# Kernel tuning notes

Measured on AMD Instinct MI355X. Metric: run time of the kernel, lower is better.

## Reference

```python
import jax, jax.numpy as jnp
import numpy as np

LN_EPS = 1e-5


def setup_inputs() -> dict:
    key = jax.random.key(0)
    ks = jax.random.split(key, 6)
    N, E, D = 100000, 600000, 128
    x = jax.random.normal(ks[0], (N, D), dtype=jnp.float32)
    edge_index = jax.random.randint(ks[1], (2, E), 0, N, dtype=jnp.int64)
    dropout_mask = jax.random.uniform(ks[2], (N, D), dtype=jnp.float32)
    ln_gamma = jnp.ones((D,), dtype=jnp.float32)
    ln_beta = jnp.zeros((D,), dtype=jnp.float32)
    W_l = jax.random.normal(ks[3], (D, D), dtype=jnp.float32) / np.sqrt(D)
    b_l = jnp.zeros((D,), dtype=jnp.float32)
    W_r = jax.random.normal(ks[4], (D, D), dtype=jnp.float32) / np.sqrt(D)
    return {"x": x, "edge_index": edge_index, "dropout_mask": dropout_mask,
            "ln_gamma": ln_gamma, "ln_beta": ln_beta,
            "W_l": W_l, "b_l": b_l, "W_r": W_r}


def reference(x, edge_index, dropout_mask, ln_gamma, ln_beta, W_l, b_l, W_r):
    N = x.shape[0]
    # LayerNorm (elementwise affine) -> ReLU -> dropout mask
    mu = jnp.mean(x, axis=-1, keepdims=True)
    var = jnp.mean(jnp.square(x - mu), axis=-1, keepdims=True)
    h = (x - mu) * jax.lax.rsqrt(var + LN_EPS) * ln_gamma + ln_beta
    h = jax.nn.relu(h) * dropout_mask  # [N, D]
    # SAGEConv with mean aggregation: messages flow src -> dst
    src, dst = edge_index[0], edge_index[1]
    agg = jax.ops.segment_sum(h[src], dst, num_segments=N)  # [N, D]
    cnt = jax.ops.segment_sum(jnp.ones_like(dst, dtype=h.dtype), dst,
                              num_segments=N)
    mean_agg = agg / jnp.maximum(cnt, 1.0)[:, None]
    # out = lin_l(mean_agg) + lin_r(h); PyG stores weights as [out, in]
    return mean_agg @ W_l.T + b_l + h @ W_r.T
```

## Files before the change

### kernel.cpp

```cpp
#include <hip/hip_runtime.h>

#define LN_EPS 1e-5f
#define D 128
#define SCAN_CHUNK 1024
#define LDSA_STRIDE 264

typedef __attribute__((ext_vector_type(4))) float f32x4;
typedef __attribute__((ext_vector_type(8))) short bf16x8;

static __device__ __forceinline__ ushort f2bf(float f) {
    union { float f; unsigned u; } a; a.f = f;
    unsigned r = a.u + 0x7FFF + ((a.u >> 16) & 1);
    return (ushort)(r >> 16);
}
static __device__ __forceinline__ float bf2f(ushort u) {
    union { unsigned u; float f; } a; a.u = ((unsigned)u) << 16;
    return a.f;
}

__global__ void prep_w(const float* __restrict__ Wl,
                       const float* __restrict__ Wr,
                       ushort* __restrict__ Bfrag,
                       int* __restrict__ hist, int N) {
    int t = blockIdx.x * blockDim.x + threadIdx.x;
    if (t < 8 * 8 * 64 * 8) {
        int i    = t & 7;
        int lane = (t >> 3) & 63;
        int jb   = (t >> 9) & 7;
        int ks   = t >> 12;
        int k = ks * 32 + (lane >> 4) * 8 + i;
        int j = jb * 16 + (lane & 15);
        float v = (k < D) ? Wl[j * D + k] : Wr[j * D + (k - D)];
        Bfrag[t] = f2bf(v);
    }
    for (int i = t; i < N; i += gridDim.x * blockDim.x) hist[i] = 0;
}

__global__ void ln_hist(const float* __restrict__ x,
                        const float* __restrict__ mask,
                        const float* __restrict__ gamma,
                        const float* __restrict__ beta,
                        ushort* __restrict__ hbf,
                        const int* __restrict__ ei,
                        int* __restrict__ hist,
                        int N, int E, int histBlocks) {
    if ((int)blockIdx.x < histBlocks) {
        int e = blockIdx.x * blockDim.x + threadIdx.x;
        if (e < E) atomicAdd(&hist[ei[E + e]], 1);
        return;
    }
    int lane = threadIdx.x & 63;
    int wid  = (((int)blockIdx.x - histBlocks) * (int)blockDim.x + (int)threadIdx.x) >> 6;
    int node = wid * 2 + (lane >> 5);
    if (node >= N) return;
    int sl = lane & 31;
    f32x4 v = ((const f32x4*)(x + (size_t)node * D))[sl];
    float s  = v.x + v.y + v.z + v.w;
    float ss = v.x * v.x + v.y * v.y + v.z * v.z + v.w * v.w;
#pragma unroll
    for (int off = 16; off > 0; off >>= 1) {
        s  += __shfl_xor(s, off);
        ss += __shfl_xor(ss, off);
    }
    float mu  = s * (1.0f / D);
    float var = ss * (1.0f / D) - mu * mu;
    float rs  = rsqrtf(var + LN_EPS);
    f32x4 g = ((const f32x4*)gamma)[sl];
    f32x4 b = ((const f32x4*)beta)[sl];
    f32x4 m = ((const f32x4*)(mask + (size_t)node * D))[sl];
    ushort4 o;
    o.x = f2bf(fmaxf((v.x - mu) * rs * g.x + b.x, 0.0f) * m.x);
    o.y = f2bf(fmaxf((v.y - mu) * rs * g.y + b.y, 0.0f) * m.y);
    o.z = f2bf(fmaxf((v.z - mu) * rs * g.z + b.z, 0.0f) * m.z);
    o.w = f2bf(fmaxf((v.w - mu) * rs * g.w + b.w, 0.0f) * m.w);
    ((ushort4*)(hbf + (size_t)node * D))[sl] = o;
}

__global__ void scan1(const int* __restrict__ hist, int* __restrict__ offs,
                      int* __restrict__ chunk_sums, int N) {
    __shared__ int lds[256];
    int base = blockIdx.x * SCAN_CHUNK;
    int t = threadIdx.x;
    int idx0 = base + t * 4;
    int v[4];
#pragma unroll
    for (int i = 0; i < 4; i++) {
        int idx = idx0 + i;
        v[i] = (idx < N) ? hist[idx] : 0;
    }
    lds[t] = v[0] + v[1] + v[2] + v[3];
    __syncthreads();
    for (int off = 1; off < 256; off <<= 1) {
        int add = (t >= off) ? lds[t - off] : 0;
        __syncthreads();
        lds[t] += add;
        __syncthreads();
    }
    int run = (t == 0) ? 0 : lds[t - 1];
    if (t == 255) chunk_sums[blockIdx.x] = lds[255];
#pragma unroll
    for (int i = 0; i < 4; i++) {
        int idx = idx0 + i;
        if (idx < N) offs[idx] = run;
        run += v[i];
    }
}

__global__ void scan_fix(int* __restrict__ offs, const int* __restrict__ csums,
                         int* __restrict__ cursor, int N) {
    __shared__ int base_s;
    int chunk = (blockIdx.x * 256) / SCAN_CHUNK;
    int t = threadIdx.x;
    if (t < 64) {
        int v = 0;
        for (int c = t; c < chunk; c += 64) v += csums[c];
#pragma unroll
        for (int off = 32; off > 0; off >>= 1) v += __shfl_xor(v, off);
        if (t == 0) base_s = v;
    }
    __syncthreads();
    int i = blockIdx.x * 256 + t;
    if (i >= N) return;
    int v = offs[i] + base_s;
    offs[i] = v;
    cursor[i] = v;
}

__global__ void sort_edges(const int* __restrict__ ei, int* __restrict__ cursor,
                           int* __restrict__ sorted_src, int E) {
    int e = blockIdx.x * blockDim.x + threadIdx.x;
    if (e >= E) return;
    int dst = ei[E + e];
    int pos = atomicAdd(&cursor[dst], 1);
    sorted_src[pos] = ei[e];
}

__global__ void __launch_bounds__(256, 3)
agg_gemm(float* __restrict__ out,
         const ushort* __restrict__ hbf,
         const int* __restrict__ sorted_src,
         const int* __restrict__ offs,
         const int* __restrict__ hist,
         const ushort* __restrict__ Bfrag,
         const float* __restrict__ bl,
         int N) {
    __shared__ ushort Alds[64 * LDSA_STRIDE];
    int tid  = threadIdx.x;
    int wave = tid >> 6;
    int lane = tid & 63;
    int n0 = blockIdx.x * 64;

#pragma unroll
    for (int it = 0; it < 4; it++) {
        int chunk = tid + 256 * it;
        int row = chunk >> 4;
        int c8  = chunk & 15;
        int node = n0 + row;
        bf16x8 vh = (bf16x8){0,0,0,0,0,0,0,0};
        if (node < N) vh = *(const bf16x8*)(hbf + (size_t)node * D + c8 * 8);
        *(bf16x8*)&Alds[row * LDSA_STRIDE + 128 + c8 * 8] = vh;
    }

    int g  = lane >> 4;
    int sl = lane & 15;
    int row0 = wave * 16 + g;
    int startp[4], degp[4];
#pragma unroll
    for (int p = 0; p < 4; p++) {
        int node = n0 + row0 + p * 4;
        startp[p] = 0; degp[p] = 0;
        if (node < N) { startp[p] = offs[node]; degp[p] = hist[node]; }
    }
    float acc[4][8];
#pragma unroll
    for (int p = 0; p < 4; p++)
#pragma unroll
        for (int q = 0; q < 8; q++) acc[p][q] = 0.0f;
    int dmax = max(max(degp[0], degp[1]), max(degp[2], degp[3]));
    for (int j = 0; j < dmax; j++) {
#pragma unroll
        for (int p = 0; p < 4; p++) {
            if (j < degp[p]) {
                int s0 = sorted_src[startp[p] + j];
                bf16x8 v = *(const bf16x8*)(hbf + (size_t)s0 * D + sl * 8);
#pragma unroll
                for (int q = 0; q < 8; q++) acc[p][q] += bf2f((ushort)v[q]);
            }
        }
    }
#pragma unroll
    for (int p = 0; p < 4; p++) {
        float inv = 1.0f / fmaxf((float)degp[p], 1.0f);
        bf16x8 o;
#pragma unroll
        for (int q = 0; q < 8; q++) o[q] = (short)f2bf(acc[p][q] * inv);
        *(bf16x8*)&Alds[(row0 + p * 4) * LDSA_STRIDE + sl * 8] = o;
    }
    __syncthreads();

    bf16x8 breg[8][2];
#pragma unroll
    for (int ks = 0; ks < 8; ks++)
#pragma unroll
        for (int jj = 0; jj < 2; jj++) {
            int jb = wave * 2 + jj;
            breg[ks][jj] = *(const bf16x8*)(Bfrag + (size_t)((ks * 8 + jb) * 64 + lane) * 8);
        }

    f32x4 acc2[4][2];
#pragma unroll
    for (int nb = 0; nb < 4; nb++)
#pragma unroll
        for (int jj = 0; jj < 2; jj++)
            acc2[nb][jj] = (f32x4){0.f, 0.f, 0.f, 0.f};

    int arow = lane & 15;
    int akoff = (lane >> 4) * 8;
#pragma unroll
    for (int ks = 0; ks < 8; ks++) {
#pragma unroll
        for (int nb = 0; nb < 4; nb++) {
            bf16x8 a = *(const bf16x8*)&Alds[(nb * 16 + arow) * LDSA_STRIDE + ks * 32 + akoff];
            acc2[nb][0] = __builtin_amdgcn_mfma_f32_16x16x32_bf16(a, breg[ks][0], acc2[nb][0], 0, 0, 0);
            acc2[nb][1] = __builtin_amdgcn_mfma_f32_16x16x32_bf16(a, breg[ks][1], acc2[nb][1], 0, 0, 0);
        }
    }

    float bias0 = bl[wave * 32 + (lane & 15)];
    float bias1 = bl[wave * 32 + 16 + (lane & 15)];
    int rbase = (lane >> 4) * 4;
#pragma unroll
    for (int nb = 0; nb < 4; nb++) {
#pragma unroll
        for (int r = 0; r < 4; r++) {
            int row = nb * 16 + rbase + r;
            if (n0 + row < N) {
                float* orow = out + (size_t)(n0 + row) * D + wave * 32 + (lane & 15);
                orow[0]  = acc2[nb][0][r] + bias0;
                orow[16] = acc2[nb][1][r] + bias1;
            }
        }
    }
}

extern "C" void kernel_launch(void* const* d_in, const int* in_sizes, int n_in,
                              void* d_out, int out_size, void* d_ws, size_t ws_size,
                              hipStream_t stream) {
    const float* x     = (const float*)d_in[0];
    const int*   ei    = (const int*)  d_in[1];
    const float* mask  = (const float*)d_in[2];
    const float* gamma = (const float*)d_in[3];
    const float* beta  = (const float*)d_in[4];
    const float* Wl    = (const float*)d_in[5];
    const float* bl    = (const float*)d_in[6];
    const float* Wr    = (const float*)d_in[7];
    float* out = (float*)d_out;

    int N = in_sizes[0] / D;
    int E = in_sizes[1] / 2;
    int chunks = (N + SCAN_CHUNK - 1) / SCAN_CHUNK;

    ushort* hbf   = (ushort*)d_ws;
    ushort* Bfrag = hbf + (size_t)N * D;
    int* hist   = (int*)(Bfrag + 32768);
    int* offs   = hist + N;
    int* cursor = offs + N;
    int* csums  = cursor + N;
    int* ssrc   = csums + 128;

    int histBlocks = (E + 255) / 256;
    int lnBlocks = (N + 7) / 8;

    prep_w<<<512, 256, 0, stream>>>(Wl, Wr, Bfrag, hist, N);
    ln_hist<<<histBlocks + lnBlocks, 256, 0, stream>>>(x, mask, gamma, beta, hbf,
                                                       ei, hist, N, E, histBlocks);
    scan1<<<chunks, 256, 0, stream>>>(hist, offs, csums, N);
    scan_fix<<<(N + 255) / 256, 256, 0, stream>>>(offs, csums, cursor, N);
    sort_edges<<<(E + 255) / 256, 256, 0, stream>>>(ei, cursor, ssrc, E);
    agg_gemm<<<(N + 63) / 64, 256, 0, stream>>>(out, hbf, ssrc, offs, hist, Bfrag, bl, N);
}
```

Measured before the change: 286.6 us.

## Fuse scan passes with lookback, merge edge sort into LayerNorm kernel, prefetch neighbor indices

Replaces the two-kernel offset scan with a single kernel. Each block publishes its flagged chunk sum and spins on the sums of earlier chunks to get its base offset. The edge counting-sort scatter now runs inside the LayerNorm launch, and the histogram uses vectorized int4 loads, cutting the number of kernel launches. The aggregation loop processes two neighbors per iteration and prefetches the next indices, using clamped loads with zero-weight masking instead of branches. Occupancy for that kernel is raised to 4 blocks per CU. The spin-wait assumes all scan blocks can be co-resident, and the masked loads add some redundant gathers.

```diff
diff --git a/kernel.cpp b/kernel.cpp
--- a/kernel.cpp
+++ b/kernel.cpp
@@ -21,7 +21,8 @@
 __global__ void prep_w(const float* __restrict__ Wl,
                        const float* __restrict__ Wr,
                        ushort* __restrict__ Bfrag,
-                       int* __restrict__ hist, int N) {
+                       int* __restrict__ hist,
+                       int* __restrict__ csums, int N) {
     int t = blockIdx.x * blockDim.x + threadIdx.x;
     if (t < 8 * 8 * 64 * 8) {
         int i    = t & 7;
@@ -33,24 +34,97 @@
         float v = (k < D) ? Wl[j * D + k] : Wr[j * D + (k - D)];
         Bfrag[t] = f2bf(v);
     }
+    if (t < 128) csums[t] = 0;
     for (int i = t; i < N; i += gridDim.x * blockDim.x) hist[i] = 0;
 }
 
-__global__ void ln_hist(const float* __restrict__ x,
+__global__ void hist_k(const int* __restrict__ ei, int* __restrict__ hist, int E) {
+    int base = (blockIdx.x * blockDim.x + threadIdx.x) * 4;
+    const int* dst = ei + E;
+    if (base + 3 < E) {
+        int4 d = *(const int4*)(dst + base);
+        atomicAdd(&hist[d.x], 1);
+        atomicAdd(&hist[d.y], 1);
+        atomicAdd(&hist[d.z], 1);
+        atomicAdd(&hist[d.w], 1);
+    } else {
+        for (int i = base; i < E && i < base + 4; i++) atomicAdd(&hist[dst[i]], 1);
+    }
+}
+
+__global__ void scan_all(const int* __restrict__ hist, int* __restrict__ offs,
+                         int* __restrict__ cursor, int* __restrict__ csums, int N) {
+    __shared__ int lds[256];
+    __shared__ int base_s;
+    int base = blockIdx.x * SCAN_CHUNK;
+    int t = threadIdx.x;
+    int idx0 = base + t * 4;
+    int v[4];
+#pragma unroll
+    for (int i = 0; i < 4; i++) {
+        int idx = idx0 + i;
+        v[i] = (idx < N) ? hist[idx] : 0;
+    }
+    lds[t] = v[0] + v[1] + v[2] + v[3];
+    __syncthreads();
+    for (int off = 1; off < 256; off <<= 1) {
+        int add = (t >= off) ? lds[t - off] : 0;
+        __syncthreads();
+        lds[t] += add;
+        __syncthreads();
+    }
+    int run = (t == 0) ? 0 : lds[t - 1];
+    if (t == 255)
+        __hip_atomic_store(&csums[blockIdx.x], lds[255] | 0x40000000,
+                           __ATOMIC_RELEASE, __HIP_MEMORY_SCOPE_AGENT);
+    if (t < 64) {
+        int b = (int)blockIdx.x;
+        int acc = 0;
+        for (int c = t; c < b; c += 64) {
+            int w;
+            do {
+                w = __hip_atomic_load(&csums[c], __ATOMIC_ACQUIRE,
+                                      __HIP_MEMORY_SCOPE_AGENT);
+            } while (!(w & 0x40000000));
+            acc += w & 0x3FFFFFFF;
+        }
+#pragma unroll
+        for (int off = 32; off > 0; off >>= 1) acc += __shfl_xor(acc, off);
+        if (t == 0) base_s = acc;
+    }
+    __syncthreads();
+    run += base_s;
+#pragma unroll
+    for (int i = 0; i < 4; i++) {
+        int idx = idx0 + i;
+        if (idx < N) {
+            offs[idx] = run;
+            cursor[idx] = run;
+        }
+        run += v[i];
+    }
+}
+
+__global__ void ln_sort(const float* __restrict__ x,
                         const float* __restrict__ mask,
                         const float* __restrict__ gamma,
                         const float* __restrict__ beta,
                         ushort* __restrict__ hbf,
                         const int* __restrict__ ei,
-                        int* __restrict__ hist,
-                        int N, int E, int histBlocks) {
-    if ((int)blockIdx.x < histBlocks) {
-        int e = blockIdx.x * blockDim.x + threadIdx.x;
-        if (e < E) atomicAdd(&hist[ei[E + e]], 1);
+                        int* __restrict__ cursor,
+                        int* __restrict__ sorted_src,
+                        int N, int E, int lnBlocks) {
+    if ((int)blockIdx.x >= lnBlocks) {
+        int e = ((int)blockIdx.x - lnBlocks) * (int)blockDim.x + (int)threadIdx.x;
+        if (e < E) {
+            int dst = ei[E + e];
+            int pos = atomicAdd(&cursor[dst], 1);
+            sorted_src[pos] = ei[e];
+        }
         return;
     }
     int lane = threadIdx.x & 63;
-    int wid  = (((int)blockIdx.x - histBlocks) * (int)blockDim.x + (int)threadIdx.x) >> 6;
+    int wid  = ((int)blockIdx.x * (int)blockDim.x + (int)threadIdx.x) >> 6;
     int node = wid * 2 + (lane >> 5);
     if (node >= N) return;
     int sl = lane & 31;
@@ -76,66 +150,7 @@
     ((ushort4*)(hbf + (size_t)node * D))[sl] = o;
 }
 
-__global__ void scan1(const int* __restrict__ hist, int* __restrict__ offs,
-                      int* __restrict__ chunk_sums, int N) {
-    __shared__ int lds[256];
-    int base = blockIdx.x * SCAN_CHUNK;
-    int t = threadIdx.x;
-    int idx0 = base + t * 4;
-    int v[4];
-#pragma unroll
-    for (int i = 0; i < 4; i++) {
-        int idx = idx0 + i;
-        v[i] = (idx < N) ? hist[idx] : 0;
-    }
-    lds[t] = v[0] + v[1] + v[2] + v[3];
-    __syncthreads();
-    for (int off = 1; off < 256; off <<= 1) {
-        int add = (t >= off) ? lds[t - off] : 0;
-        __syncthreads();
-        lds[t] += add;
-        __syncthreads();
-    }
-    int run = (t == 0) ? 0 : lds[t - 1];
-    if (t == 255) chunk_sums[blockIdx.x] = lds[255];
-#pragma unroll
-    for (int i = 0; i < 4; i++) {
-        int idx = idx0 + i;
-        if (idx < N) offs[idx] = run;
-        run += v[i];
-    }
-}
-
-__global__ void scan_fix(int* __restrict__ offs, const int* __restrict__ csums,
-                         int* __restrict__ cursor, int N) {
-    __shared__ int base_s;
-    int chunk = (blockIdx.x * 256) / SCAN_CHUNK;
-    int t = threadIdx.x;
-    if (t < 64) {
-        int v = 0;
-        for (int c = t; c < chunk; c += 64) v += csums[c];
-#pragma unroll
-        for (int off = 32; off > 0; off >>= 1) v += __shfl_xor(v, off);
-        if (t == 0) base_s = v;
-    }
-    __syncthreads();
-    int i = blockIdx.x * 256 + t;
-    if (i >= N) return;
-    int v = offs[i] + base_s;
-    offs[i] = v;
-    cursor[i] = v;
-}
-
-__global__ void sort_edges(const int* __restrict__ ei, int* __restrict__ cursor,
-                           int* __restrict__ sorted_src, int E) {
-    int e = blockIdx.x * blockDim.x + threadIdx.x;
-    if (e >= E) return;
-    int dst = ei[E + e];
-    int pos = atomicAdd(&cursor[dst], 1);
-    sorted_src[pos] = ei[e];
-}
-
-__global__ void __launch_bounds__(256, 3)
+__global__ void __launch_bounds__(256, 4)
 agg_gemm(float* __restrict__ out,
          const ushort* __restrict__ hbf,
          const int* __restrict__ sorted_src,
@@ -143,7 +158,7 @@
          const int* __restrict__ hist,
          const ushort* __restrict__ Bfrag,
          const float* __restrict__ bl,
-         int N) {
+         int N, int E) {
     __shared__ ushort Alds[64 * LDSA_STRIDE];
     int tid  = threadIdx.x;
     int wave = tid >> 6;
@@ -164,33 +179,62 @@
     int g  = lane >> 4;
     int sl = lane & 15;
     int row0 = wave * 16 + g;
-    int startp[4], degp[4];
+    int start[4], deg[4], dm1[4];
 #pragma unroll
     for (int p = 0; p < 4; p++) {
         int node = n0 + row0 + p * 4;
-        startp[p] = 0; degp[p] = 0;
-        if (node < N) { startp[p] = offs[node]; degp[p] = hist[node]; }
+        start[p] = 0; deg[p] = 0;
+        if (node < N) { start[p] = offs[node]; deg[p] = hist[node]; }
+        dm1[p] = deg[p] - 1; if (dm1[p] < 0) dm1[p] = 0;
     }
     float acc[4][8];
 #pragma unroll
     for (int p = 0; p < 4; p++)
 #pragma unroll
         for (int q = 0; q < 8; q++) acc[p][q] = 0.0f;
-    int dmax = max(max(degp[0], degp[1]), max(degp[2], degp[3]));
-    for (int j = 0; j < dmax; j++) {
+
+    int dmax = max(max(deg[0], deg[1]), max(deg[2], deg[3]));
+    int Em = E - 1;
+    int ia[4], ib[4];
+#pragma unroll
+    for (int p = 0; p < 4; p++) {
+        int pa = start[p];                         if (pa > Em) pa = Em;
+        int j1 = (1 < dm1[p]) ? 1 : dm1[p];
+        int pb = start[p] + j1;                    if (pb > Em) pb = Em;
+        ia[p] = sorted_src[pa];
+        ib[p] = sorted_src[pb];
+    }
+    for (int j = 0; j < dmax; j += 2) {
+        int ca[4], cb[4];
+#pragma unroll
+        for (int p = 0; p < 4; p++) { ca[p] = ia[p]; cb[p] = ib[p]; }
 #pragma unroll
         for (int p = 0; p < 4; p++) {
-            if (j < degp[p]) {
-                int s0 = sorted_src[startp[p] + j];
-                bf16x8 v = *(const bf16x8*)(hbf + (size_t)s0 * D + sl * 8);
-#pragma unroll
-                for (int q = 0; q < 8; q++) acc[p][q] += bf2f((ushort)v[q]);
-            }
+            int j2 = (j + 2 < dm1[p]) ? j + 2 : dm1[p];
+            int j3 = (j + 3 < dm1[p]) ? j + 3 : dm1[p];
+            int pa = start[p] + j2; if (pa > Em) pa = Em;
+            int pb = start[p] + j3; if (pb > Em) pb = Em;
+            ia[p] = sorted_src[pa];
+            ib[p] = sorted_src[pb];
+        }
+#pragma unroll
+        for (int p = 0; p < 4; p++) {
+            bf16x8 v = *(const bf16x8*)(hbf + (size_t)ca[p] * D + sl * 8);
+            float m = (j < deg[p]) ? 1.0f : 0.0f;
+#pragma unroll
+            for (int q = 0; q < 8; q++) acc[p][q] += bf2f((ushort)v[q]) * m;
+        }
+#pragma unroll
+        for (int p = 0; p < 4; p++) {
+            bf16x8 v = *(const bf16x8*)(hbf + (size_t)cb[p] * D + sl * 8);
+            float m = (j + 1 < deg[p]) ? 1.0f : 0.0f;
+#pragma unroll
+            for (int q = 0; q < 8; q++) acc[p][q] += bf2f((ushort)v[q]) * m;
         }
     }
 #pragma unroll
     for (int p = 0; p < 4; p++) {
-        float inv = 1.0f / fmaxf((float)degp[p], 1.0f);
+        float inv = 1.0f / fmaxf((float)deg[p], 1.0f);
         bf16x8 o;
 #pragma unroll
         for (int q = 0; q < 8; q++) o[q] = (short)f2bf(acc[p][q] * inv);
@@ -268,14 +312,14 @@
     int* csums  = cursor + N;
     int* ssrc   = csums + 128;
 
-    int histBlocks = (E + 255) / 256;
-    int lnBlocks = (N + 7) / 8;
-
-    prep_w<<<512, 256, 0, stream>>>(Wl, Wr, Bfrag, hist, N);
-    ln_hist<<<histBlocks + lnBlocks, 256, 0, stream>>>(x, mask, gamma, beta, hbf,
-                                                       ei, hist, N, E, histBlocks);
-    scan1<<<chunks, 256, 0, stream>>>(hist, offs, csums, N);
-    scan_fix<<<(N + 255) / 256, 256, 0, stream>>>(offs, csums, cursor, N);
-    sort_edges<<<(E + 255) / 256, 256, 0, stream>>>(ei, cursor, ssrc, E);
-    agg_gemm<<<(N + 63) / 64, 256, 0, stream>>>(out, hbf, ssrc, offs, hist, Bfrag, bl, N);
-}
+    int lnBlocks   = (N + 7) / 8;
+    int sortBlocks = (E + 255) / 256;
+
+    prep_w<<<512, 256, 0, stream>>>(Wl, Wr, Bfrag, hist, csums, N);
+    hist_k<<<(E / 4 + 255) / 256, 256, 0, stream>>>(ei, hist, E);
+    scan_all<<<chunks, 256, 0, stream>>>(hist, offs, cursor, csums, N);
+    ln_sort<<<lnBlocks + sortBlocks, 256, 0, stream>>>(x, mask, gamma, beta, hbf,
+                                                       ei, cursor, ssrc, N, E, lnBlocks);
+    agg_gemm<<<(N + 63) / 64, 256, 0, stream>>>(out, hbf, ssrc, offs, hist, Bfrag,
+                                                bl, N, E);
+}
```

After: 256.9 us. 1.12x faster.
